# Kernel optimization log

Measured on AMD Instinct MI355X. Metric: run time of the kernel, lower is better.

## Reference

```python
import jax, jax.numpy as jnp
import numpy as np
from jax import lax

EPS = 1e-5


def setup_inputs() -> dict:
    key = jax.random.key(0)
    ks = jax.random.split(key, 6)
    n, c, t, v, K = 64, 256, 64, 25, 3
    c4 = c // 4
    x = jax.random.normal(ks[0], (n, c, t, v), dtype=jnp.float32)
    # G branch: Linear(t -> 2t, no bias), BN1d(2t), Linear(2t -> K, no bias)
    Wg1 = jax.random.normal(ks[1], (2 * t, t), dtype=jnp.float32) * 0.1
    gamma1 = jnp.ones((2 * t,), jnp.float32)
    beta1 = jnp.zeros((2 * t,), jnp.float32)
    mean1 = jnp.zeros((2 * t,), jnp.float32)
    var1 = jnp.ones((2 * t,), jnp.float32)
    Wg2 = jax.random.normal(ks[2], (K, 2 * t), dtype=jnp.float32) * 0.1
    # L branch: Conv1d(c -> c/4, k=3, pad=1, no bias), BN1d(c/4), Conv1d(c/4 -> c, k=1, no bias)
    WL1 = jax.random.normal(ks[3], (c4, c, K), dtype=jnp.float32) * 0.05
    gamma2 = jnp.ones((c4,), jnp.float32)
    beta2 = jnp.zeros((c4,), jnp.float32)
    mean2 = jnp.zeros((c4,), jnp.float32)
    var2 = jnp.ones((c4,), jnp.float32)
    WL2 = jax.random.normal(ks[4], (c, c4, 1), dtype=jnp.float32) * 0.05
    return {"x": x, "Wg1": Wg1, "gamma1": gamma1, "beta1": beta1, "mean1": mean1,
            "var1": var1, "Wg2": Wg2, "WL1": WL1, "gamma2": gamma2, "beta2": beta2,
            "mean2": mean2, "var2": var2, "WL2": WL2}


def _bn(h, gamma, beta, mean, var):
    return (h - mean) * gamma * lax.rsqrt(var + EPS) + beta


def reference(x, Wg1, gamma1, beta1, mean1, var1, Wg2, WL1, gamma2, beta2, mean2, var2, WL2):
    n, c, t, v = x.shape
    K = Wg2.shape[0]
    pad = 1  # module default padding (temporal)
    # adaptive_avg_pool2d(x, (t, 1)) == mean over joints v -> (n, c, t)
    pooled = x.mean(axis=-1)
    # --- G: per-(n,c) temporal kernel via MLP + softmax ---
    h = pooled.reshape(n * c, t) @ Wg1.T                  # (n*c, 2t)
    h = jax.nn.relu(_bn(h, gamma1, beta1, mean1, var1))
    kern = jax.nn.softmax(h @ Wg2.T, axis=-1)             # (n*c, K)
    kern = kern.reshape(n, c, K)
    # --- L: channel-wise local activation (conv1d over t) ---
    dn = ('NCH', 'OIH', 'NCH')
    a = lax.conv_general_dilated(pooled, WL1, (1,), [(K // 2, K // 2)], dimension_numbers=dn)
    a = jax.nn.relu(_bn(a, gamma2[None, :, None], beta2[None, :, None],
                        mean2[None, :, None], var2[None, :, None]))
    a = lax.conv_general_dilated(a, WL2, (1,), [(0, 0)], dimension_numbers=dn)
    act = jax.nn.sigmoid(a)                               # (n, c, t)
    new_x = x * act[..., None]                            # (n, c, t, v)
    # --- dynamic depthwise temporal conv (groups = n*c) ---
    xp = jnp.pad(new_x, ((0, 0), (0, 0), (pad, pad), (0, 0)))
    out = jnp.zeros_like(x)
    for k in range(K):  # K is tiny (3)
        out = out + kern[:, :, k, None, None] * xp[:, :, k:k + t, :]
    return out + x
```

## Files before the change

kernel.cpp:

```cpp
#include <hip/hip_runtime.h>
#include <math.h>

#define EPSB 1e-5f

constexpr int N_ = 64, C_ = 256, T_ = 64, V_ = 25, C4_ = 64;
constexpr int NC = N_ * C_;
constexpr int TV = T_ * V_;

__global__ __launch_bounds__(256) void k_pool(const float* __restrict__ x,
                                              float* __restrict__ pooled) {
    __shared__ float xs[4 * TV];
    const int b = blockIdx.x;
    const float* xp = x + (size_t)b * (4 * TV);
    for (int e = threadIdx.x; e < 4 * TV; e += 256) xs[e] = xp[e];
    __syncthreads();
    float s = 0.f;
    const int base = threadIdx.x * V_;
#pragma unroll
    for (int v = 0; v < V_; ++v) s += xs[base + v];
    pooled[(size_t)b * 256 + threadIdx.x] = s * (1.0f / 25.0f);
}

__global__ __launch_bounds__(256) void k_gbranch(
    const float* __restrict__ pooled, const float* __restrict__ Wg1,
    const float* __restrict__ g1, const float* __restrict__ b1,
    const float* __restrict__ m1, const float* __restrict__ v1,
    const float* __restrict__ Wg2, float* __restrict__ kern,
    int rows_per_wave) {
    const int lane = threadIdx.x & 63;
    const int gw = blockIdx.x * (blockDim.x >> 6) + (threadIdx.x >> 6);
    const int j0 = lane, j1 = lane + 64;

    float w0[T_], w1[T_];
#pragma unroll
    for (int t = 0; t < T_; ++t) {
        w0[t] = Wg1[j0 * T_ + t];
        w1[t] = Wg1[j1 * T_ + t];
    }
    const float s0 = g1[j0] * rsqrtf(v1[j0] + EPSB);
    const float s1 = g1[j1] * rsqrtf(v1[j1] + EPSB);
    const float c0 = b1[j0] - m1[j0] * s0;
    const float c1 = b1[j1] - m1[j1] * s1;
    const float wa0 = Wg2[0 * 128 + j0], wa1 = Wg2[0 * 128 + j1];
    const float wb0 = Wg2[1 * 128 + j0], wb1 = Wg2[1 * 128 + j1];
    const float wc0 = Wg2[2 * 128 + j0], wc1 = Wg2[2 * 128 + j1];

    for (int rr = 0; rr < rows_per_wave; ++rr) {
        const int row = gw * rows_per_wave + rr;
        const float pv = pooled[(size_t)row * T_ + lane];
        float h0 = 0.f, h1 = 0.f;
#pragma unroll
        for (int t = 0; t < T_; ++t) {
            const float pt = __shfl(pv, t);
            h0 = fmaf(w0[t], pt, h0);
            h1 = fmaf(w1[t], pt, h1);
        }
        h0 = fmaxf(fmaf(h0, s0, c0), 0.f);
        h1 = fmaxf(fmaf(h1, s1, c1), 0.f);
        float p0 = wa0 * h0 + wa1 * h1;
        float p1 = wb0 * h0 + wb1 * h1;
        float p2 = wc0 * h0 + wc1 * h1;
#pragma unroll
        for (int off = 32; off > 0; off >>= 1) {
            p0 += __shfl_xor(p0, off);
            p1 += __shfl_xor(p1, off);
            p2 += __shfl_xor(p2, off);
        }
        const float mx = fmaxf(p0, fmaxf(p1, p2));
        const float e0 = expf(p0 - mx), e1 = expf(p1 - mx), e2 = expf(p2 - mx);
        const float inv = 1.0f / (e0 + e1 + e2);
        if (lane < 3) {
            const float val = (lane == 0) ? e0 : (lane == 1) ? e1 : e2;
            kern[(size_t)row * 3 + lane] = val * inv;
        }
    }
}

__global__ __launch_bounds__(256) void k_lbranch(
    const float* __restrict__ pooled, const float* __restrict__ WL1,
    const float* __restrict__ g2, const float* __restrict__ b2,
    const float* __restrict__ m2, const float* __restrict__ v2,
    const float* __restrict__ WL2, float* __restrict__ act) {
    __shared__ float ps[C_][18];
    __shared__ float a1s[C4_][17];
    const int nb = blockIdx.x;
    const int n = nb >> 2;
    const int t0 = (nb & 3) * 16;
    const float* pn = pooled + (size_t)n * C_ * T_;

    for (int e = threadIdx.x; e < C_ * 18; e += 256) {
        const int i = e / 18, tt = e % 18;
        const int gt = t0 - 1 + tt;
        ps[i][tt] = (gt >= 0 && gt < T_) ? pn[i * T_ + gt] : 0.f;
    }
    __syncthreads();

    const int cc = threadIdx.x >> 2;
    const int tt0 = (threadIdx.x & 3) * 4;
    float a0 = 0.f, a1 = 0.f, a2 = 0.f, a3 = 0.f;
    const float* wrow = WL1 + (size_t)cc * C_ * 3;
    for (int i = 0; i < C_; ++i) {
        const float wk0 = wrow[i * 3 + 0];
        const float wk1 = wrow[i * 3 + 1];
        const float wk2 = wrow[i * 3 + 2];
        const float pA = ps[i][tt0 + 0], pB = ps[i][tt0 + 1];
        const float pC = ps[i][tt0 + 2], pD = ps[i][tt0 + 3];
        const float pE = ps[i][tt0 + 4], pF = ps[i][tt0 + 5];
        a0 = fmaf(wk0, pA, fmaf(wk1, pB, fmaf(wk2, pC, a0)));
        a1 = fmaf(wk0, pB, fmaf(wk1, pC, fmaf(wk2, pD, a1)));
        a2 = fmaf(wk0, pC, fmaf(wk1, pD, fmaf(wk2, pE, a2)));
        a3 = fmaf(wk0, pD, fmaf(wk1, pE, fmaf(wk2, pF, a3)));
    }
    const float sc = g2[cc] * rsqrtf(v2[cc] + EPSB);
    const float sh = b2[cc] - m2[cc] * sc;
    a1s[cc][tt0 + 0] = fmaxf(fmaf(a0, sc, sh), 0.f);
    a1s[cc][tt0 + 1] = fmaxf(fmaf(a1, sc, sh), 0.f);
    a1s[cc][tt0 + 2] = fmaxf(fmaf(a2, sc, sh), 0.f);
    a1s[cc][tt0 + 3] = fmaxf(fmaf(a3, sc, sh), 0.f);
    __syncthreads();

    const int c = threadIdx.x;
    float o[16];
#pragma unroll
    for (int q = 0; q < 16; ++q) o[q] = 0.f;
    const float* w2 = WL2 + (size_t)c * C4_;
    for (int i = 0; i < C4_; ++i) {
        const float w = w2[i];
#pragma unroll
        for (int q = 0; q < 16; ++q) o[q] = fmaf(w, a1s[i][q], o[q]);
    }
    float* arow = act + ((size_t)n * C_ + c) * T_ + t0;
#pragma unroll
    for (int q = 0; q < 16; ++q) arow[q] = 1.0f / (1.0f + expf(-o[q]));
}

__global__ __launch_bounds__(256) void k_final(const float* __restrict__ x,
                                               const float* __restrict__ act,
                                               const float* __restrict__ kern,
                                               float* __restrict__ out) {
    __shared__ float xs[TV];
    __shared__ float as[T_ + 2];
    const int row = blockIdx.x;
    const float* xr = x + (size_t)row * TV;
    float* outr = out + (size_t)row * TV;
    for (int e = threadIdx.x; e < TV; e += 256) xs[e] = xr[e];
    if (threadIdx.x < T_ + 2) {
        const int t = (int)threadIdx.x - 1;
        as[threadIdx.x] = (t >= 0 && t < T_) ? act[(size_t)row * T_ + t] : 0.f;
    }
    const float k0 = kern[(size_t)row * 3 + 0];
    const float k1 = kern[(size_t)row * 3 + 1];
    const float k2 = kern[(size_t)row * 3 + 2];
    __syncthreads();
    for (int e = threadIdx.x; e < TV; e += 256) {
        const int t = e / 25;
        const float xc = xs[e];
        const float xm = (t > 0)  ? xs[e - 25] : 0.f;
        const float xq = (t < 63) ? xs[e + 25] : 0.f;
        outr[e] = xc + k0 * xm * as[t] + k1 * xc * as[t + 1] + k2 * xq * as[t + 2];
    }
}

extern "C" void kernel_launch(void* const* d_in, const int* in_sizes, int n_in,
                              void* d_out, int out_size, void* d_ws, size_t ws_size,
                              hipStream_t stream) {
    const float* x   = (const float*)d_in[0];
    const float* Wg1 = (const float*)d_in[1];
    const float* g1  = (const float*)d_in[2];
    const float* b1  = (const float*)d_in[3];
    const float* m1  = (const float*)d_in[4];
    const float* v1  = (const float*)d_in[5];
    const float* Wg2 = (const float*)d_in[6];
    const float* WL1 = (const float*)d_in[7];
    const float* g2  = (const float*)d_in[8];
    const float* b2  = (const float*)d_in[9];
    const float* m2  = (const float*)d_in[10];
    const float* v2  = (const float*)d_in[11];
    const float* WL2 = (const float*)d_in[12];
    float* out = (float*)d_out;

    float* ws = (float*)d_ws;
    float* pooled = ws;
    float* act    = ws + (size_t)NC * T_;
    float* kern   = ws + (size_t)2 * NC * T_;

    k_pool   <<<NC / 4, 256, 0, stream>>>(x, pooled);
    k_gbranch<<<512,    256, 0, stream>>>(pooled, Wg1, g1, b1, m1, v1, Wg2, kern, 8);
    k_lbranch<<<N_ * 4, 256, 0, stream>>>(pooled, WL1, g2, b2, m2, v2, WL2, act);
    k_final  <<<NC,     256, 0, stream>>>(x, act, kern, out);
}
```

Before: 283.6 us.

## Vectorize pool/final loads, stage Wg1 in LDS, split L-branch into two kernels

The pool and final kernels now use float4 global loads and stores. The G-branch transposes Wg1 into shared memory for coalesced weight loads and reads pooled rows through wave-uniform scalar loads instead of shuffles. The L-branch is split into two kernels: a conv kernel where each wave computes 4 output channels across all 64 timesteps using scalar weight loads, and a 1x1-conv+sigmoid kernel launched with more blocks. The split adds a launch and a round trip of an intermediate buffer through global memory.

```diff
diff --git a/kernel.cpp b/kernel.cpp
--- a/kernel.cpp
+++ b/kernel.cpp
@@ -11,8 +11,9 @@
                                               float* __restrict__ pooled) {
     __shared__ float xs[4 * TV];
     const int b = blockIdx.x;
-    const float* xp = x + (size_t)b * (4 * TV);
-    for (int e = threadIdx.x; e < 4 * TV; e += 256) xs[e] = xp[e];
+    const float4* xp4 = (const float4*)(x + (size_t)b * (4 * TV));
+    float4* xs4 = (float4*)xs;
+    for (int f = threadIdx.x; f < TV; f += 256) xs4[f] = xp4[f];
     __syncthreads();
     float s = 0.f;
     const int base = threadIdx.x * V_;
@@ -25,17 +26,23 @@
     const float* __restrict__ pooled, const float* __restrict__ Wg1,
     const float* __restrict__ g1, const float* __restrict__ b1,
     const float* __restrict__ m1, const float* __restrict__ v1,
-    const float* __restrict__ Wg2, float* __restrict__ kern,
-    int rows_per_wave) {
+    const float* __restrict__ Wg2, float* __restrict__ kern) {
+    __shared__ float Wt[T_ * 130];
+    for (int e = threadIdx.x; e < 128 * T_; e += 256) {
+        const int j = e >> 6, t = e & 63;
+        Wt[t * 130 + j] = Wg1[e];
+    }
+    __syncthreads();
+
     const int lane = threadIdx.x & 63;
-    const int gw = blockIdx.x * (blockDim.x >> 6) + (threadIdx.x >> 6);
+    const int gw = blockIdx.x * 4 + (threadIdx.x >> 6);
     const int j0 = lane, j1 = lane + 64;
 
     float w0[T_], w1[T_];
 #pragma unroll
     for (int t = 0; t < T_; ++t) {
-        w0[t] = Wg1[j0 * T_ + t];
-        w1[t] = Wg1[j1 * T_ + t];
+        w0[t] = Wt[t * 130 + j0];
+        w1[t] = Wt[t * 130 + j1];
     }
     const float s0 = g1[j0] * rsqrtf(v1[j0] + EPSB);
     const float s1 = g1[j1] * rsqrtf(v1[j1] + EPSB);
@@ -45,13 +52,13 @@
     const float wb0 = Wg2[1 * 128 + j0], wb1 = Wg2[1 * 128 + j1];
     const float wc0 = Wg2[2 * 128 + j0], wc1 = Wg2[2 * 128 + j1];
 
-    for (int rr = 0; rr < rows_per_wave; ++rr) {
-        const int row = gw * rows_per_wave + rr;
-        const float pv = pooled[(size_t)row * T_ + lane];
+    for (int rr = 0; rr < 8; ++rr) {
+        const int row = __builtin_amdgcn_readfirstlane(gw * 8 + rr);
+        const float* __restrict__ prow = pooled + (size_t)row * T_;
         float h0 = 0.f, h1 = 0.f;
 #pragma unroll
         for (int t = 0; t < T_; ++t) {
-            const float pt = __shfl(pv, t);
+            const float pt = prow[t];
             h0 = fmaf(w0[t], pt, h0);
             h1 = fmaf(w1[t], pt, h1);
         }
@@ -76,62 +83,77 @@
     }
 }
 
-__global__ __launch_bounds__(256) void k_lbranch(
+__global__ __launch_bounds__(256) void kL1(
     const float* __restrict__ pooled, const float* __restrict__ WL1,
     const float* __restrict__ g2, const float* __restrict__ b2,
     const float* __restrict__ m2, const float* __restrict__ v2,
-    const float* __restrict__ WL2, float* __restrict__ act) {
-    __shared__ float ps[C_][18];
-    __shared__ float a1s[C4_][17];
-    const int nb = blockIdx.x;
-    const int n = nb >> 2;
-    const int t0 = (nb & 3) * 16;
-    const float* pn = pooled + (size_t)n * C_ * T_;
-
-    for (int e = threadIdx.x; e < C_ * 18; e += 256) {
-        const int i = e / 18, tt = e % 18;
-        const int gt = t0 - 1 + tt;
-        ps[i][tt] = (gt >= 0 && gt < T_) ? pn[i * T_ + gt] : 0.f;
-    }
-    __syncthreads();
-
-    const int cc = threadIdx.x >> 2;
-    const int tt0 = (threadIdx.x & 3) * 4;
-    float a0 = 0.f, a1 = 0.f, a2 = 0.f, a3 = 0.f;
-    const float* wrow = WL1 + (size_t)cc * C_ * 3;
+    float* __restrict__ a1) {
+    __shared__ float ps[C_ * 66];
+    const int n = blockIdx.x >> 2;
+    const int bq = blockIdx.x & 3;
+    const int w = threadIdx.x >> 6;
+    const int t = threadIdx.x & 63;
+    const float* pn = pooled + (size_t)n * (C_ * T_);
+
+    for (int e = threadIdx.x; e < C_ * T_; e += 256) {
+        const int i = e >> 6, tt = e & 63;
+        ps[i * 66 + 1 + tt] = pn[e];
+    }
+    {
+        const int i = threadIdx.x;
+        ps[i * 66] = 0.f;
+        ps[i * 66 + 65] = 0.f;
+    }
+    __syncthreads();
+
+    const int ccb = __builtin_amdgcn_readfirstlane(bq * 16 + w * 4);
+    const float* __restrict__ wb = WL1 + (size_t)ccb * (C_ * 3);
+    float a0 = 0.f, a1v = 0.f, a2 = 0.f, a3 = 0.f;
+#pragma unroll 4
     for (int i = 0; i < C_; ++i) {
-        const float wk0 = wrow[i * 3 + 0];
-        const float wk1 = wrow[i * 3 + 1];
-        const float wk2 = wrow[i * 3 + 2];
-        const float pA = ps[i][tt0 + 0], pB = ps[i][tt0 + 1];
-        const float pC = ps[i][tt0 + 2], pD = ps[i][tt0 + 3];
-        const float pE = ps[i][tt0 + 4], pF = ps[i][tt0 + 5];
-        a0 = fmaf(wk0, pA, fmaf(wk1, pB, fmaf(wk2, pC, a0)));
-        a1 = fmaf(wk0, pB, fmaf(wk1, pC, fmaf(wk2, pD, a1)));
-        a2 = fmaf(wk0, pC, fmaf(wk1, pD, fmaf(wk2, pE, a2)));
-        a3 = fmaf(wk0, pD, fmaf(wk1, pE, fmaf(wk2, pF, a3)));
-    }
-    const float sc = g2[cc] * rsqrtf(v2[cc] + EPSB);
-    const float sh = b2[cc] - m2[cc] * sc;
-    a1s[cc][tt0 + 0] = fmaxf(fmaf(a0, sc, sh), 0.f);
-    a1s[cc][tt0 + 1] = fmaxf(fmaf(a1, sc, sh), 0.f);
-    a1s[cc][tt0 + 2] = fmaxf(fmaf(a2, sc, sh), 0.f);
-    a1s[cc][tt0 + 3] = fmaxf(fmaf(a3, sc, sh), 0.f);
-    __syncthreads();
-
-    const int c = threadIdx.x;
-    float o[16];
-#pragma unroll
-    for (int q = 0; q < 16; ++q) o[q] = 0.f;
-    const float* w2 = WL2 + (size_t)c * C4_;
+        const float pm = ps[i * 66 + t];
+        const float pc = ps[i * 66 + 1 + t];
+        const float pp = ps[i * 66 + 2 + t];
+        a0 = fmaf(wb[0 * 768 + i * 3 + 0], pm, fmaf(wb[0 * 768 + i * 3 + 1], pc, fmaf(wb[0 * 768 + i * 3 + 2], pp, a0)));
+        a1v = fmaf(wb[1 * 768 + i * 3 + 0], pm, fmaf(wb[1 * 768 + i * 3 + 1], pc, fmaf(wb[1 * 768 + i * 3 + 2], pp, a1v)));
+        a2 = fmaf(wb[2 * 768 + i * 3 + 0], pm, fmaf(wb[2 * 768 + i * 3 + 1], pc, fmaf(wb[2 * 768 + i * 3 + 2], pp, a2)));
+        a3 = fmaf(wb[3 * 768 + i * 3 + 0], pm, fmaf(wb[3 * 768 + i * 3 + 1], pc, fmaf(wb[3 * 768 + i * 3 + 2], pp, a3)));
+    }
+    float* ab = a1 + ((size_t)n * C4_ + ccb) * T_ + t;
+    const float acc[4] = {a0, a1v, a2, a3};
+#pragma unroll
+    for (int j = 0; j < 4; ++j) {
+        const int cc = ccb + j;
+        const float sc = g2[cc] * rsqrtf(v2[cc] + EPSB);
+        const float sh = b2[cc] - m2[cc] * sc;
+        ab[j * T_] = fmaxf(fmaf(acc[j], sc, sh), 0.f);
+    }
+}
+
+__global__ __launch_bounds__(256) void kL2(
+    const float* __restrict__ a1, const float* __restrict__ WL2,
+    float* __restrict__ act) {
+    const int n = blockIdx.x >> 4;
+    const int bq = blockIdx.x & 15;
+    const int w = threadIdx.x >> 6;
+    const int t = threadIdx.x & 63;
+    const int cb = __builtin_amdgcn_readfirstlane(bq * 16 + w * 4);
+    const float* __restrict__ an = a1 + (size_t)n * (C4_ * T_);
+    const float* __restrict__ w2 = WL2 + (size_t)cb * C4_;
+    float o0 = 0.f, o1 = 0.f, o2 = 0.f, o3 = 0.f;
+#pragma unroll 4
     for (int i = 0; i < C4_; ++i) {
-        const float w = w2[i];
-#pragma unroll
-        for (int q = 0; q < 16; ++q) o[q] = fmaf(w, a1s[i][q], o[q]);
-    }
-    float* arow = act + ((size_t)n * C_ + c) * T_ + t0;
-#pragma unroll
-    for (int q = 0; q < 16; ++q) arow[q] = 1.0f / (1.0f + expf(-o[q]));
+        const float av = an[i * T_ + t];
+        o0 = fmaf(w2[0 * C4_ + i], av, o0);
+        o1 = fmaf(w2[1 * C4_ + i], av, o1);
+        o2 = fmaf(w2[2 * C4_ + i], av, o2);
+        o3 = fmaf(w2[3 * C4_ + i], av, o3);
+    }
+    float* ar = act + ((size_t)n * C_ + cb) * T_ + t;
+    ar[0 * T_] = 1.0f / (1.0f + expf(-o0));
+    ar[1 * T_] = 1.0f / (1.0f + expf(-o1));
+    ar[2 * T_] = 1.0f / (1.0f + expf(-o2));
+    ar[3 * T_] = 1.0f / (1.0f + expf(-o3));
 }
 
 __global__ __launch_bounds__(256) void k_final(const float* __restrict__ x,
@@ -141,9 +163,10 @@
     __shared__ float xs[TV];
     __shared__ float as[T_ + 2];
     const int row = blockIdx.x;
-    const float* xr = x + (size_t)row * TV;
-    float* outr = out + (size_t)row * TV;
-    for (int e = threadIdx.x; e < TV; e += 256) xs[e] = xr[e];
+    const float4* xr4 = (const float4*)(x + (size_t)row * TV);
+    float4* outr4 = (float4*)(out + (size_t)row * TV);
+    float4* xs4 = (float4*)xs;
+    for (int f = threadIdx.x; f < TV / 4; f += 256) xs4[f] = xr4[f];
     if (threadIdx.x < T_ + 2) {
         const int t = (int)threadIdx.x - 1;
         as[threadIdx.x] = (t >= 0 && t < T_) ? act[(size_t)row * T_ + t] : 0.f;
@@ -152,12 +175,18 @@
     const float k1 = kern[(size_t)row * 3 + 1];
     const float k2 = kern[(size_t)row * 3 + 2];
     __syncthreads();
-    for (int e = threadIdx.x; e < TV; e += 256) {
-        const int t = e / 25;
-        const float xc = xs[e];
-        const float xm = (t > 0)  ? xs[e - 25] : 0.f;
-        const float xq = (t < 63) ? xs[e + 25] : 0.f;
-        outr[e] = xc + k0 * xm * as[t] + k1 * xc * as[t + 1] + k2 * xq * as[t + 2];
+    for (int f = threadIdx.x; f < TV / 4; f += 256) {
+        float r[4];
+#pragma unroll
+        for (int q = 0; q < 4; ++q) {
+            const int e = f * 4 + q;
+            const int t = e / 25;
+            const float xc = xs[e];
+            const float xm = (t > 0)  ? xs[e - 25] : 0.f;
+            const float xq = (t < 63) ? xs[e + 25] : 0.f;
+            r[q] = xc + k0 * xm * as[t] + k1 * xc * as[t + 1] + k2 * xq * as[t + 2];
+        }
+        outr4[f] = make_float4(r[0], r[1], r[2], r[3]);
     }
 }
 
@@ -183,9 +212,11 @@
     float* pooled = ws;
     float* act    = ws + (size_t)NC * T_;
     float* kern   = ws + (size_t)2 * NC * T_;
+    float* a1buf  = ws + (size_t)2 * NC * T_ + (size_t)NC * 4;
 
     k_pool   <<<NC / 4, 256, 0, stream>>>(x, pooled);
-    k_gbranch<<<512,    256, 0, stream>>>(pooled, Wg1, g1, b1, m1, v1, Wg2, kern, 8);
-    k_lbranch<<<N_ * 4, 256, 0, stream>>>(pooled, WL1, g2, b2, m2, v2, WL2, act);
+    k_gbranch<<<512,    256, 0, stream>>>(pooled, Wg1, g1, b1, m1, v1, Wg2, kern);
+    kL1      <<<N_ * 4, 256, 0, stream>>>(pooled, WL1, g2, b2, m2, v2, a1buf);
+    kL2      <<<N_ * 16,256, 0, stream>>>(a1buf, WL2, act);
     k_final  <<<NC,     256, 0, stream>>>(x, act, kern, out);
 }
```

New measurement: 279.3 us. No clear change (-1.5%).

## Merge G and L branches into one kernel and vectorize pool/final passes

Applied to the files above, without the earlier changes.

Combines the G-branch MLP and L-branch conv kernels into a single launch that dispatches on block index, dropping one kernel launch. The G path now stages Wg1 transposed in shared memory and processes 8 rows per wave with readlane broadcasts instead of shuffles. The L path uses finer time tiles so more blocks run. The pool and final kernels switch to float4 loads, and the final kernel handles 4 rows per block with nontemporal vector stores. This targets launch overhead, register pressure, and memory bandwidth, at the cost of larger shared memory use and a more complex indexing scheme.

```diff
diff --git a/kernel.cpp b/kernel.cpp
--- a/kernel.cpp
+++ b/kernel.cpp
@@ -2,6 +2,8 @@
 #include <math.h>
 
 #define EPSB 1e-5f
+
+typedef float f32x4 __attribute__((ext_vector_type(4)));
 
 constexpr int N_ = 64, C_ = 256, T_ = 64, V_ = 25, C4_ = 64;
 constexpr int NC = N_ * C_;
@@ -11,8 +13,9 @@
                                               float* __restrict__ pooled) {
     __shared__ float xs[4 * TV];
     const int b = blockIdx.x;
-    const float* xp = x + (size_t)b * (4 * TV);
-    for (int e = threadIdx.x; e < 4 * TV; e += 256) xs[e] = xp[e];
+    const float4* xp4 = (const float4*)(x + (size_t)b * (4 * TV));
+    float4* xs4 = (float4*)xs;
+    for (int f = threadIdx.x; f < TV; f += 256) xs4[f] = xp4[f];
     __syncthreads();
     float s = 0.f;
     const int base = threadIdx.x * V_;
@@ -21,143 +24,177 @@
     pooled[(size_t)b * 256 + threadIdx.x] = s * (1.0f / 25.0f);
 }
 
-__global__ __launch_bounds__(256) void k_gbranch(
-    const float* __restrict__ pooled, const float* __restrict__ Wg1,
-    const float* __restrict__ g1, const float* __restrict__ b1,
-    const float* __restrict__ m1, const float* __restrict__ v1,
-    const float* __restrict__ Wg2, float* __restrict__ kern,
-    int rows_per_wave) {
-    const int lane = threadIdx.x & 63;
-    const int gw = blockIdx.x * (blockDim.x >> 6) + (threadIdx.x >> 6);
-    const int j0 = lane, j1 = lane + 64;
-
-    float w0[T_], w1[T_];
-#pragma unroll
-    for (int t = 0; t < T_; ++t) {
-        w0[t] = Wg1[j0 * T_ + t];
-        w1[t] = Wg1[j1 * T_ + t];
+union GLsm {
+    float Wt[64 * 130];
+    struct { float ps[C_ * 10]; float a1s[C4_ * 9]; } L;
+};
+
+__global__ __launch_bounds__(256) void k_GL(
+    const float* __restrict__ pooled,
+    const float* __restrict__ Wg1, const float* __restrict__ g1,
+    const float* __restrict__ b1, const float* __restrict__ m1,
+    const float* __restrict__ v1, const float* __restrict__ Wg2,
+    const float* __restrict__ WL1, const float* __restrict__ g2,
+    const float* __restrict__ b2, const float* __restrict__ m2,
+    const float* __restrict__ v2, const float* __restrict__ WL2,
+    float* __restrict__ kern, float* __restrict__ act) {
+    __shared__ GLsm sm;
+    const int tid = threadIdx.x, bid = blockIdx.x;
+    const int lane = tid & 63, wv = tid >> 6;
+
+    if (bid < 512) {
+        for (int e = tid; e < 128 * 64; e += 256) {
+            const int j = e >> 6, t = e & 63;
+            sm.Wt[t * 130 + j] = Wg1[e];
+        }
+        __syncthreads();
+        const int j0 = lane, j1 = lane + 64;
+        const float s0 = g1[j0] * rsqrtf(v1[j0] + EPSB);
+        const float s1 = g1[j1] * rsqrtf(v1[j1] + EPSB);
+        const float c0 = b1[j0] - m1[j0] * s0;
+        const float c1 = b1[j1] - m1[j1] * s1;
+        const float wa0 = Wg2[j0], wa1 = Wg2[j1];
+        const float wb0 = Wg2[128 + j0], wb1 = Wg2[128 + j1];
+        const float wc0 = Wg2[256 + j0], wc1 = Wg2[256 + j1];
+
+        const int r0 = (bid * 4 + wv) * 8;
+        float pv[8], h0[8], h1[8];
+#pragma unroll
+        for (int r = 0; r < 8; ++r) {
+            pv[r] = pooled[(size_t)(r0 + r) * 64 + lane];
+            h0[r] = 0.f; h1[r] = 0.f;
+        }
+#pragma unroll
+        for (int tb = 0; tb < 4; ++tb) {
+            float w0[16], w1[16];
+#pragma unroll
+            for (int tt = 0; tt < 16; ++tt) {
+                w0[tt] = sm.Wt[(tb * 16 + tt) * 130 + j0];
+                w1[tt] = sm.Wt[(tb * 16 + tt) * 130 + j1];
+            }
+#pragma unroll
+            for (int tt = 0; tt < 16; ++tt) {
+#pragma unroll
+                for (int r = 0; r < 8; ++r) {
+                    const float pt = __uint_as_float(
+                        __builtin_amdgcn_readlane(__float_as_uint(pv[r]), tb * 16 + tt));
+                    h0[r] = fmaf(w0[tt], pt, h0[r]);
+                    h1[r] = fmaf(w1[tt], pt, h1[r]);
+                }
+            }
+        }
+#pragma unroll
+        for (int r = 0; r < 8; ++r) {
+            const float a0 = fmaxf(fmaf(h0[r], s0, c0), 0.f);
+            const float a1v = fmaxf(fmaf(h1[r], s1, c1), 0.f);
+            float p0 = wa0 * a0 + wa1 * a1v;
+            float p1 = wb0 * a0 + wb1 * a1v;
+            float p2 = wc0 * a0 + wc1 * a1v;
+#pragma unroll
+            for (int off = 32; off > 0; off >>= 1) {
+                p0 += __shfl_xor(p0, off);
+                p1 += __shfl_xor(p1, off);
+                p2 += __shfl_xor(p2, off);
+            }
+            const float mx = fmaxf(p0, fmaxf(p1, p2));
+            const float e0 = expf(p0 - mx), e1 = expf(p1 - mx), e2 = expf(p2 - mx);
+            const float inv = 1.0f / (e0 + e1 + e2);
+            if (lane < 3) {
+                const float val = (lane == 0) ? e0 : (lane == 1) ? e1 : e2;
+                kern[(size_t)(r0 + r) * 3 + lane] = val * inv;
+            }
+        }
+    } else {
+        const int Lb = bid - 512;
+        const int n = Lb >> 3;
+        const int t0 = (Lb & 7) * 8;
+        for (int e = tid; e < C_ * 10; e += 256) {
+            const int i = e / 10, tt = e - i * 10;
+            const int gt = t0 - 1 + tt;
+            sm.L.ps[e] = (gt >= 0 && gt < 64)
+                             ? pooled[(size_t)n * 16384 + i * 64 + gt] : 0.f;
+        }
+        __syncthreads();
+        const int cc = tid >> 2;
+        const int tq = tid & 3;
+        float acc0 = 0.f, acc1 = 0.f;
+        const float* __restrict__ wrow = WL1 + (size_t)cc * 768;
+#pragma unroll 4
+        for (int i = 0; i < C_; ++i) {
+            const float pA = sm.L.ps[i * 10 + 2 * tq + 0];
+            const float pB = sm.L.ps[i * 10 + 2 * tq + 1];
+            const float pC = sm.L.ps[i * 10 + 2 * tq + 2];
+            const float pD = sm.L.ps[i * 10 + 2 * tq + 3];
+            const float wk0 = wrow[i * 3 + 0];
+            const float wk1 = wrow[i * 3 + 1];
+            const float wk2 = wrow[i * 3 + 2];
+            acc0 = fmaf(wk0, pA, fmaf(wk1, pB, fmaf(wk2, pC, acc0)));
+            acc1 = fmaf(wk0, pB, fmaf(wk1, pC, fmaf(wk2, pD, acc1)));
+        }
+        const float sc = g2[cc] * rsqrtf(v2[cc] + EPSB);
+        const float sh = b2[cc] - m2[cc] * sc;
+        sm.L.a1s[cc * 9 + 2 * tq + 0] = fmaxf(fmaf(acc0, sc, sh), 0.f);
+        sm.L.a1s[cc * 9 + 2 * tq + 1] = fmaxf(fmaf(acc1, sc, sh), 0.f);
+        __syncthreads();
+        const int c = tid;
+        float o[8];
+#pragma unroll
+        for (int q = 0; q < 8; ++q) o[q] = 0.f;
+        const float* __restrict__ w2 = WL2 + (size_t)c * 64;
+#pragma unroll 4
+        for (int i = 0; i < C4_; ++i) {
+            const float w = w2[i];
+#pragma unroll
+            for (int q = 0; q < 8; ++q)
+                o[q] = fmaf(w, sm.L.a1s[i * 9 + q], o[q]);
+        }
+        float* ar = act + ((size_t)n * 256 + c) * 64 + t0;
+#pragma unroll
+        for (int q = 0; q < 8; ++q) ar[q] = 1.0f / (1.0f + expf(-o[q]));
     }
-    const float s0 = g1[j0] * rsqrtf(v1[j0] + EPSB);
-    const float s1 = g1[j1] * rsqrtf(v1[j1] + EPSB);
-    const float c0 = b1[j0] - m1[j0] * s0;
-    const float c1 = b1[j1] - m1[j1] * s1;
-    const float wa0 = Wg2[0 * 128 + j0], wa1 = Wg2[0 * 128 + j1];
-    const float wb0 = Wg2[1 * 128 + j0], wb1 = Wg2[1 * 128 + j1];
-    const float wc0 = Wg2[2 * 128 + j0], wc1 = Wg2[2 * 128 + j1];
-
-    for (int rr = 0; rr < rows_per_wave; ++rr) {
-        const int row = gw * rows_per_wave + rr;
-        const float pv = pooled[(size_t)row * T_ + lane];
-        float h0 = 0.f, h1 = 0.f;
-#pragma unroll
-        for (int t = 0; t < T_; ++t) {
-            const float pt = __shfl(pv, t);
-            h0 = fmaf(w0[t], pt, h0);
-            h1 = fmaf(w1[t], pt, h1);
-        }
-        h0 = fmaxf(fmaf(h0, s0, c0), 0.f);
-        h1 = fmaxf(fmaf(h1, s1, c1), 0.f);
-        float p0 = wa0 * h0 + wa1 * h1;
-        float p1 = wb0 * h0 + wb1 * h1;
-        float p2 = wc0 * h0 + wc1 * h1;
-#pragma unroll
-        for (int off = 32; off > 0; off >>= 1) {
-            p0 += __shfl_xor(p0, off);
-            p1 += __shfl_xor(p1, off);
-            p2 += __shfl_xor(p2, off);
-        }
-        const float mx = fmaxf(p0, fmaxf(p1, p2));
-        const float e0 = expf(p0 - mx), e1 = expf(p1 - mx), e2 = expf(p2 - mx);
-        const float inv = 1.0f / (e0 + e1 + e2);
-        if (lane < 3) {
-            const float val = (lane == 0) ? e0 : (lane == 1) ? e1 : e2;
-            kern[(size_t)row * 3 + lane] = val * inv;
-        }
-    }
-}
-
-__global__ __launch_bounds__(256) void k_lbranch(
-    const float* __restrict__ pooled, const float* __restrict__ WL1,
-    const float* __restrict__ g2, const float* __restrict__ b2,
-    const float* __restrict__ m2, const float* __restrict__ v2,
-    const float* __restrict__ WL2, float* __restrict__ act) {
-    __shared__ float ps[C_][18];
-    __shared__ float a1s[C4_][17];
-    const int nb = blockIdx.x;
-    const int n = nb >> 2;
-    const int t0 = (nb & 3) * 16;
-    const float* pn = pooled + (size_t)n * C_ * T_;
-
-    for (int e = threadIdx.x; e < C_ * 18; e += 256) {
-        const int i = e / 18, tt = e % 18;
-        const int gt = t0 - 1 + tt;
-        ps[i][tt] = (gt >= 0 && gt < T_) ? pn[i * T_ + gt] : 0.f;
-    }
-    __syncthreads();
-
-    const int cc = threadIdx.x >> 2;
-    const int tt0 = (threadIdx.x & 3) * 4;
-    float a0 = 0.f, a1 = 0.f, a2 = 0.f, a3 = 0.f;
-    const float* wrow = WL1 + (size_t)cc * C_ * 3;
-    for (int i = 0; i < C_; ++i) {
-        const float wk0 = wrow[i * 3 + 0];
-        const float wk1 = wrow[i * 3 + 1];
-        const float wk2 = wrow[i * 3 + 2];
-        const float pA = ps[i][tt0 + 0], pB = ps[i][tt0 + 1];
-        const float pC = ps[i][tt0 + 2], pD = ps[i][tt0 + 3];
-        const float pE = ps[i][tt0 + 4], pF = ps[i][tt0 + 5];
-        a0 = fmaf(wk0, pA, fmaf(wk1, pB, fmaf(wk2, pC, a0)));
-        a1 = fmaf(wk0, pB, fmaf(wk1, pC, fmaf(wk2, pD, a1)));
-        a2 = fmaf(wk0, pC, fmaf(wk1, pD, fmaf(wk2, pE, a2)));
-        a3 = fmaf(wk0, pD, fmaf(wk1, pE, fmaf(wk2, pF, a3)));
-    }
-    const float sc = g2[cc] * rsqrtf(v2[cc] + EPSB);
-    const float sh = b2[cc] - m2[cc] * sc;
-    a1s[cc][tt0 + 0] = fmaxf(fmaf(a0, sc, sh), 0.f);
-    a1s[cc][tt0 + 1] = fmaxf(fmaf(a1, sc, sh), 0.f);
-    a1s[cc][tt0 + 2] = fmaxf(fmaf(a2, sc, sh), 0.f);
-    a1s[cc][tt0 + 3] = fmaxf(fmaf(a3, sc, sh), 0.f);
-    __syncthreads();
-
-    const int c = threadIdx.x;
-    float o[16];
-#pragma unroll
-    for (int q = 0; q < 16; ++q) o[q] = 0.f;
-    const float* w2 = WL2 + (size_t)c * C4_;
-    for (int i = 0; i < C4_; ++i) {
-        const float w = w2[i];
-#pragma unroll
-        for (int q = 0; q < 16; ++q) o[q] = fmaf(w, a1s[i][q], o[q]);
-    }
-    float* arow = act + ((size_t)n * C_ + c) * T_ + t0;
-#pragma unroll
-    for (int q = 0; q < 16; ++q) arow[q] = 1.0f / (1.0f + expf(-o[q]));
 }
 
 __global__ __launch_bounds__(256) void k_final(const float* __restrict__ x,
                                                const float* __restrict__ act,
                                                const float* __restrict__ kern,
                                                float* __restrict__ out) {
-    __shared__ float xs[TV];
-    __shared__ float as[T_ + 2];
-    const int row = blockIdx.x;
-    const float* xr = x + (size_t)row * TV;
-    float* outr = out + (size_t)row * TV;
-    for (int e = threadIdx.x; e < TV; e += 256) xs[e] = xr[e];
-    if (threadIdx.x < T_ + 2) {
-        const int t = (int)threadIdx.x - 1;
-        as[threadIdx.x] = (t >= 0 && t < T_) ? act[(size_t)row * T_ + t] : 0.f;
+    __shared__ float xs[4 * TV];
+    __shared__ float as[4 * 66];
+    __shared__ float ks[12];
+    const int b = blockIdx.x;
+    const int r0 = b * 4;
+    const float4* xr4 = (const float4*)(x + (size_t)b * (4 * TV));
+    float4* xs4 = (float4*)xs;
+    for (int f = threadIdx.x; f < TV; f += 256) xs4[f] = xr4[f];
+    for (int e = threadIdx.x; e < 4 * 66; e += 256) {
+        const int row = e / 66, tt = e - row * 66;
+        const int t = tt - 1;
+        as[e] = (t >= 0 && t < 64) ? act[(size_t)(r0 + row) * 64 + t] : 0.f;
     }
-    const float k0 = kern[(size_t)row * 3 + 0];
-    const float k1 = kern[(size_t)row * 3 + 1];
-    const float k2 = kern[(size_t)row * 3 + 2];
+    if (threadIdx.x < 12) ks[threadIdx.x] = kern[(size_t)b * 12 + threadIdx.x];
     __syncthreads();
-    for (int e = threadIdx.x; e < TV; e += 256) {
-        const int t = e / 25;
-        const float xc = xs[e];
-        const float xm = (t > 0)  ? xs[e - 25] : 0.f;
-        const float xq = (t < 63) ? xs[e + 25] : 0.f;
-        outr[e] = xc + k0 * xm * as[t] + k1 * xc * as[t + 1] + k2 * xq * as[t + 2];
+    for (int f = threadIdx.x; f < TV; f += 256) {
+        const int row = f / 400;
+        const int e0 = (f - row * 400) * 4;
+        const int rb = row * TV;
+        float r[4];
+#pragma unroll
+        for (int q = 0; q < 4; ++q) {
+            const int e = e0 + q;
+            const int t = e / 25;
+            const int idx = rb + e;
+            const float xc = xs[idx];
+            const float xm = (t > 0)  ? xs[idx - 25] : 0.f;
+            const float xq = (t < 63) ? xs[idx + 25] : 0.f;
+            const float am = as[row * 66 + t];
+            const float ac = as[row * 66 + t + 1];
+            const float ap = as[row * 66 + t + 2];
+            r[q] = fmaf(ks[row * 3 + 0], xm * am,
+                   fmaf(ks[row * 3 + 1], xc * ac,
+                   fmaf(ks[row * 3 + 2], xq * ap, xc)));
+        }
+        f32x4 v = {r[0], r[1], r[2], r[3]};
+        __builtin_nontemporal_store(v, (f32x4*)(out + (size_t)b * (4 * TV)) + f);
     }
 }
 
@@ -184,8 +221,8 @@
     float* act    = ws + (size_t)NC * T_;
     float* kern   = ws + (size_t)2 * NC * T_;
 
-    k_pool   <<<NC / 4, 256, 0, stream>>>(x, pooled);
-    k_gbranch<<<512,    256, 0, stream>>>(pooled, Wg1, g1, b1, m1, v1, Wg2, kern, 8);
-    k_lbranch<<<N_ * 4, 256, 0, stream>>>(pooled, WL1, g2, b2, m2, v2, WL2, act);
-    k_final  <<<NC,     256, 0, stream>>>(x, act, kern, out);
-}
+    k_pool <<<NC / 4, 256, 0, stream>>>(x, pooled);
+    k_GL   <<<1024,   256, 0, stream>>>(pooled, Wg1, g1, b1, m1, v1, Wg2,
+                                        WL1, g2, b2, m2, v2, WL2, kern, act);
+    k_final<<<NC / 4, 256, 0, stream>>>(x, act, kern, out);
+}
```

Measured after the change: 275.6 us. 1.03x faster.
